# Optimization experiments

Hardware: AMD Instinct MI355X
Metric: run time of the kernel (lower is better)

Reference implementation:

```python
import math
import jax, jax.numpy as jnp
import numpy as np

DEGREE = 5
LN_EPS = 1e-5


def hermite_psi(C, r):
    # x_d = tanh(linspace(-1,1,C)) * (sqrt(2r+1)+1), shape [C]
    x_d = jnp.tanh(jnp.linspace(-1.0, 1.0, C)) * (math.sqrt(2 * r + 1) + 1.0)
    g = jnp.exp(-x_d ** 2 / 2.0)
    rows = [math.pi ** (-0.25) * g]
    if r > 0:
        rows.append(math.sqrt(2.0) * math.pi ** (-0.25) * x_d * g)
    for k in range(2, r + 1):
        rows.append(math.sqrt(2.0 / k) * x_d * rows[-1] - math.sqrt((k - 1) / k) * rows[-2])
    return jnp.stack(rows)  # [r+1, C]


def setup_inputs() -> dict:
    key = jax.random.key(0)
    k1, k2 = jax.random.split(key)
    B, C, H, W = 16, 512, 64, 64
    O = 512
    x = jax.random.normal(k1, (B, C, H, W), dtype=jnp.float32)
    ln_w = jnp.ones((C,), dtype=jnp.float32)
    ln_b = jnp.zeros((C,), dtype=jnp.float32)
    fc_w = jax.random.normal(k2, (O, C), dtype=jnp.float32) * (1.0 / math.sqrt(C))
    fc_b = jnp.zeros((O,), dtype=jnp.float32)
    return {"x": x, "ln_w": ln_w, "ln_b": ln_b, "fc_w": fc_w, "fc_b": fc_b}


def reference(x, ln_w, ln_b, fc_w, fc_b):
    B, C, H, W = x.shape
    O = fc_w.shape[0]
    # [B, HW, C]
    q = x.reshape(B, C, H * W).transpose(0, 2, 1)
    # LayerNorm over channels (biased variance, eps=1e-5)
    mu = q.mean(axis=-1, keepdims=True)
    var = ((q - mu) ** 2).mean(axis=-1, keepdims=True)
    q = (q - mu) / jnp.sqrt(var + LN_EPS) * ln_w + ln_b
    # Constant Hermite basis [r+1, C]
    psi = hermite_psi(C, DEGREE).astype(x.dtype)
    # Tiny cross-attention: scores [B, HW, r+1]
    scores = jnp.einsum('bnc,rc->bnr', q, psi) / math.sqrt(C)
    attn = jax.nn.softmax(scores, axis=-1)
    y = jnp.einsum('bnr,rc->bnc', attn, psi)  # [B, HW, C]
    # 1x1 conv == pointwise GEMM over channels
    out = jnp.einsum('bnc,oc->bon', y, fc_w) + fc_b[None, :, None]
    return out.reshape(B, O, H, W)
```

## Files before the change

kernel.cpp:

```cpp
#include <hip/hip_runtime.h>
#include <math.h>

#define C 512
#define NPIX 4096
#define BATCH 16
#define O 512
#define R 6
#define LN_EPS 1e-5f


__global__ __launch_bounds__(512) void setup_psi(const float* __restrict__ lnw,
                                                 const float* __restrict__ lnb,
                                                 float* __restrict__ ws) {
    __shared__ float sh_psi[R * C];
    const int c = threadIdx.x;
    float t = -1.0f + 2.0f * (float)c / 511.0f;
    float xd = tanhf(t) * 4.31662479035539984911f;
    float g = expf(-0.5f * xd * xd);
    const float pi_m14 = 0.75112554446494248286f;
    float rows[R];
    rows[0] = pi_m14 * g;
    rows[1] = 1.41421356237309504880f * pi_m14 * xd * g;
    #pragma unroll
    for (int k = 2; k <= 5; ++k)
        rows[k] = sqrtf(2.0f / k) * xd * rows[k - 1] - sqrtf((k - 1.0f) / k) * rows[k - 2];
    float w = lnw[c];
    #pragma unroll
    for (int r = 0; r < R; ++r) {
        sh_psi[r * C + c] = rows[r];
        ws[r * C + c] = rows[r];
        ws[3072 + r * C + c] = rows[r] * w;
    }
    __syncthreads();
    if (threadIdx.x < 12) {
        int r = (threadIdx.x < 6) ? threadIdx.x : threadIdx.x - 6;
        const float* vec = (threadIdx.x < 6) ? lnw : lnb;
        float sacc = 0.f;
        for (int c2 = 0; c2 < C; ++c2) sacc += vec[c2] * sh_psi[r * C + c2];
        ws[(threadIdx.x < 6 ? 6144 : 6152) + r] = sacc;
    }
}

__global__ __launch_bounds__(64) void setup_M(const float* __restrict__ fcw,
                                              const float* __restrict__ fcb,
                                              float* __restrict__ ws) {
    const int o = blockIdx.x;
    const int lane = threadIdx.x;
    const float* psi = ws;
    float acc[R] = {0.f, 0.f, 0.f, 0.f, 0.f, 0.f};
    for (int c = lane; c < C; c += 64) {
        float w = fcw[o * C + c];
        #pragma unroll
        for (int r = 0; r < R; ++r) acc[r] += psi[r * C + c] * w;
    }
    #pragma unroll
    for (int r = 0; r < R; ++r)
        for (int m = 32; m >= 1; m >>= 1) acc[r] += __shfl_xor(acc[r], m, 64);
    if (lane == 0) {
        float bias = fcb[o];
        #pragma unroll
        for (int r = 0; r < R; ++r) ws[6160 + r * O + o] = acc[r] + bias;
    }
}

__global__ __launch_bounds__(256) void fused_main(const float* __restrict__ x,
                                                  const float* __restrict__ ws,
                                                  float* __restrict__ out) {
    __shared__ float sh_wpsi[R * C];
    __shared__ float sh_M[R * O];
    const int tid = threadIdx.x;
    const int b = blockIdx.x >> 4;
    const int nblk = blockIdx.x & 15;
    const int n = (nblk << 8) + tid;

    const float* wpsi_g = ws + 3072;
    const float* M_g = ws + 6160;
    for (int i = tid; i < R * C; i += 256) {
        sh_wpsi[i] = wpsi_g[i];
        sh_M[i] = M_g[i];
    }
    float swp[R], sbp[R];
    #pragma unroll
    for (int r = 0; r < R; ++r) { swp[r] = ws[6144 + r]; sbp[r] = ws[6152 + r]; }
    __syncthreads();

    const float* xb = x + (size_t)b * C * NPIX + n;
    float s = 0.f, ss = 0.f;
    float a0 = 0.f, a1 = 0.f, a2 = 0.f, a3 = 0.f, a4 = 0.f, a5 = 0.f;
    #pragma unroll 16
    for (int c = 0; c < C; ++c) {
        float xv = xb[(size_t)c * NPIX];
        s += xv;
        ss += xv * xv;
        a0 += xv * sh_wpsi[0 * C + c];
        a1 += xv * sh_wpsi[1 * C + c];
        a2 += xv * sh_wpsi[2 * C + c];
        a3 += xv * sh_wpsi[3 * C + c];
        a4 += xv * sh_wpsi[4 * C + c];
        a5 += xv * sh_wpsi[5 * C + c];
    }
    float mu = s * (1.0f / 512.0f);
    float var = ss * (1.0f / 512.0f) - mu * mu;
    float rsig = rsqrtf(var + LN_EPS);
    const float invsq = 0.04419417382415922f;

    float a[R] = {a0, a1, a2, a3, a4, a5};
    float sc[R];
    float mx = -1e30f;
    #pragma unroll
    for (int r = 0; r < R; ++r) {
        sc[r] = ((a[r] - mu * swp[r]) * rsig + sbp[r]) * invsq;
        mx = fmaxf(mx, sc[r]);
    }
    float attn[R];
    float es = 0.f;
    #pragma unroll
    for (int r = 0; r < R; ++r) { attn[r] = expf(sc[r] - mx); es += attn[r]; }
    float inv = 1.0f / es;
    #pragma unroll
    for (int r = 0; r < R; ++r) attn[r] *= inv;

    float* ob = out + (size_t)b * O * NPIX + n;
    #pragma unroll 8
    for (int o = 0; o < O; ++o) {
        float v = attn[0] * sh_M[0 * O + o] + attn[1] * sh_M[1 * O + o] +
                  attn[2] * sh_M[2 * O + o] + attn[3] * sh_M[3 * O + o] +
                  attn[4] * sh_M[4 * O + o] + attn[5] * sh_M[5 * O + o];
        ob[(size_t)o * NPIX] = v;
    }
}

extern "C" void kernel_launch(void* const* d_in, const int* in_sizes, int n_in,
                              void* d_out, int out_size, void* d_ws, size_t ws_size,
                              hipStream_t stream) {
    const float* x    = (const float*)d_in[0];
    const float* ln_w = (const float*)d_in[1];
    const float* ln_b = (const float*)d_in[2];
    const float* fc_w = (const float*)d_in[3];
    const float* fc_b = (const float*)d_in[4];
    float* out = (float*)d_out;
    float* ws = (float*)d_ws;

    setup_psi<<<1, 512, 0, stream>>>(ln_w, ln_b, ws);
    setup_M<<<O, 64, 0, stream>>>(fc_w, fc_b, ws);
    fused_main<<<BATCH * 16, 256, 0, stream>>>(x, ws, out);
}
```

Before: 278.3 us.

## Split channel reduction across waves, use more blocks and vectorized float4 stores

The main kernel now runs 1024 blocks of 64 pixels each instead of 256 blocks of 256 pixels. Within a block, the four waves each reduce a quarter of the channels and combine their partial sums through shared memory. The weighted-psi table is stored interleaved per channel so each channel needs one float4 plus one float2 shared-memory load. The output GEMM has each thread write float4 over 4 pixels for 32 output channels. The setup reduction is also parallelized with wave shuffles. The aim is more parallelism for the bandwidth-bound read and write phases, at the cost of extra barriers and shared-memory traffic.

```diff
diff --git a/kernel.cpp b/kernel.cpp
--- a/kernel.cpp
+++ b/kernel.cpp
@@ -28,16 +28,28 @@
     #pragma unroll
     for (int r = 0; r < R; ++r) {
         sh_psi[r * C + c] = rows[r];
-        ws[r * C + c] = rows[r];
-        ws[3072 + r * C + c] = rows[r] * w;
+        ws[8192 + r * C + c] = rows[r];
+        ws[c * 8 + r] = rows[r] * w;
     }
     __syncthreads();
-    if (threadIdx.x < 12) {
-        int r = (threadIdx.x < 6) ? threadIdx.x : threadIdx.x - 6;
-        const float* vec = (threadIdx.x < 6) ? lnw : lnb;
-        float sacc = 0.f;
-        for (int c2 = 0; c2 < C; ++c2) sacc += vec[c2] * sh_psi[r * C + c2];
-        ws[(threadIdx.x < 6 ? 6144 : 6152) + r] = sacc;
+    const int wv = threadIdx.x >> 6;
+    const int l = threadIdx.x & 63;
+    #pragma unroll
+    for (int pass = 0; pass < 2; ++pass) {
+        int combo = pass * 8 + wv;
+        if (combo < 12) {
+            int r = (combo < 6) ? combo : combo - 6;
+            const float* vec = (combo < 6) ? lnw : lnb;
+            float acc = 0.f;
+            #pragma unroll
+            for (int j = 0; j < 8; ++j) {
+                int cc = l + 64 * j;
+                acc += vec[cc] * sh_psi[r * C + cc];
+            }
+            #pragma unroll
+            for (int m = 32; m >= 1; m >>= 1) acc += __shfl_xor(acc, m, 64);
+            if (l == 0) ws[(combo < 6 ? 4096 : 4104) + r] = acc;
+        }
     }
 }
 
@@ -46,7 +58,7 @@
                                               float* __restrict__ ws) {
     const int o = blockIdx.x;
     const int lane = threadIdx.x;
-    const float* psi = ws;
+    const float* psi = ws + 8192;
     float acc[R] = {0.f, 0.f, 0.f, 0.f, 0.f, 0.f};
     for (int c = lane; c < C; c += 64) {
         float w = fcw[o * C + c];
@@ -59,74 +71,101 @@
     if (lane == 0) {
         float bias = fcb[o];
         #pragma unroll
-        for (int r = 0; r < R; ++r) ws[6160 + r * O + o] = acc[r] + bias;
+        for (int r = 0; r < R; ++r) ws[4112 + r * O + o] = acc[r] + bias;
     }
 }
 
-__global__ __launch_bounds__(256) void fused_main(const float* __restrict__ x,
-                                                  const float* __restrict__ ws,
-                                                  float* __restrict__ out) {
-    __shared__ float sh_wpsi[R * C];
-    __shared__ float sh_M[R * O];
+__global__ __launch_bounds__(256, 4) void fused_main(const float* __restrict__ x,
+                                                     const float* __restrict__ ws,
+                                                     float* __restrict__ out) {
+    __shared__ float shW[C * 8];
+    __shared__ float shM[R * O];
+    __shared__ float part[4][8][64];
+    __shared__ float attnS[R][64];
+
     const int tid = threadIdx.x;
-    const int b = blockIdx.x >> 4;
-    const int nblk = blockIdx.x & 15;
-    const int n = (nblk << 8) + tid;
+    const int wv = tid >> 6;
+    const int l = tid & 63;
+    const int b = blockIdx.x >> 6;
+    const int ng = blockIdx.x & 63;
+    const int n0 = ng << 6;
 
-    const float* wpsi_g = ws + 3072;
-    const float* M_g = ws + 6160;
-    for (int i = tid; i < R * C; i += 256) {
-        sh_wpsi[i] = wpsi_g[i];
-        sh_M[i] = M_g[i];
+    {
+        const float4* wsrc = (const float4*)ws;
+        float4* wdst = (float4*)shW;
+        for (int i = tid; i < 1024; i += 256) wdst[i] = wsrc[i];
+        const float4* msrc = (const float4*)(ws + 4112);
+        float4* mdst = (float4*)shM;
+        for (int i = tid; i < 768; i += 256) mdst[i] = msrc[i];
     }
-    float swp[R], sbp[R];
-    #pragma unroll
-    for (int r = 0; r < R; ++r) { swp[r] = ws[6144 + r]; sbp[r] = ws[6152 + r]; }
     __syncthreads();
 
-    const float* xb = x + (size_t)b * C * NPIX + n;
+    const float* xb = x + ((size_t)(b * C + (wv << 7)) << 12) + n0 + l;
     float s = 0.f, ss = 0.f;
     float a0 = 0.f, a1 = 0.f, a2 = 0.f, a3 = 0.f, a4 = 0.f, a5 = 0.f;
     #pragma unroll 16
-    for (int c = 0; c < C; ++c) {
-        float xv = xb[(size_t)c * NPIX];
+    for (int i = 0; i < 128; ++i) {
+        float xv = xb[(size_t)i << 12];
+        const float* wr = &shW[((wv << 7) + i) << 3];
+        float4 w03 = *(const float4*)wr;
+        float2 w45 = *(const float2*)(wr + 4);
         s += xv;
         ss += xv * xv;
-        a0 += xv * sh_wpsi[0 * C + c];
-        a1 += xv * sh_wpsi[1 * C + c];
-        a2 += xv * sh_wpsi[2 * C + c];
-        a3 += xv * sh_wpsi[3 * C + c];
-        a4 += xv * sh_wpsi[4 * C + c];
-        a5 += xv * sh_wpsi[5 * C + c];
+        a0 += xv * w03.x;
+        a1 += xv * w03.y;
+        a2 += xv * w03.z;
+        a3 += xv * w03.w;
+        a4 += xv * w45.x;
+        a5 += xv * w45.y;
     }
-    float mu = s * (1.0f / 512.0f);
-    float var = ss * (1.0f / 512.0f) - mu * mu;
-    float rsig = rsqrtf(var + LN_EPS);
-    const float invsq = 0.04419417382415922f;
+    part[wv][0][l] = s;  part[wv][1][l] = ss;
+    part[wv][2][l] = a0; part[wv][3][l] = a1;
+    part[wv][4][l] = a2; part[wv][5][l] = a3;
+    part[wv][6][l] = a4; part[wv][7][l] = a5;
+    __syncthreads();
 
-    float a[R] = {a0, a1, a2, a3, a4, a5};
-    float sc[R];
-    float mx = -1e30f;
+    if (tid < 64) {
+        float v[8];
+        #pragma unroll
+        for (int j = 0; j < 8; ++j)
+            v[j] = part[0][j][tid] + part[1][j][tid] + part[2][j][tid] + part[3][j][tid];
+        float mu = v[0] * (1.0f / 512.0f);
+        float var = v[1] * (1.0f / 512.0f) - mu * mu;
+        float rsig = rsqrtf(var + LN_EPS);
+        const float invsq = 0.04419417382415922f;
+        float sc[R], mx = -1e30f;
+        #pragma unroll
+        for (int r = 0; r < R; ++r) {
+            float swp = ws[4096 + r], sbp = ws[4104 + r];
+            sc[r] = ((v[2 + r] - mu * swp) * rsig + sbp) * invsq;
+            mx = fmaxf(mx, sc[r]);
+        }
+        float es = 0.f, at[R];
+        #pragma unroll
+        for (int r = 0; r < R; ++r) { at[r] = expf(sc[r] - mx); es += at[r]; }
+        float inv = 1.0f / es;
+        #pragma unroll
+        for (int r = 0; r < R; ++r) attnS[r][tid] = at[r] * inv;
+    }
+    __syncthreads();
+
+    const int pxg = (tid & 15) << 2;
+    const int og = tid >> 4;
+    float4 a4v[R];
     #pragma unroll
-    for (int r = 0; r < R; ++r) {
-        sc[r] = ((a[r] - mu * swp[r]) * rsig + sbp[r]) * invsq;
-        mx = fmaxf(mx, sc[r]);
-    }
-    float attn[R];
-    float es = 0.f;
-    #pragma unroll
-    for (int r = 0; r < R; ++r) { attn[r] = expf(sc[r] - mx); es += attn[r]; }
-    float inv = 1.0f / es;
-    #pragma unroll
-    for (int r = 0; r < R; ++r) attn[r] *= inv;
-
-    float* ob = out + (size_t)b * O * NPIX + n;
+    for (int r = 0; r < R; ++r) a4v[r] = *(const float4*)&attnS[r][pxg];
+    float* ob = out + ((size_t)(b * O) << 12) + n0 + pxg;
     #pragma unroll 8
-    for (int o = 0; o < O; ++o) {
-        float v = attn[0] * sh_M[0 * O + o] + attn[1] * sh_M[1 * O + o] +
-                  attn[2] * sh_M[2 * O + o] + attn[3] * sh_M[3 * O + o] +
-                  attn[4] * sh_M[4 * O + o] + attn[5] * sh_M[5 * O + o];
-        ob[(size_t)o * NPIX] = v;
+    for (int k = 0; k < 32; ++k) {
+        int o = og + (k << 4);
+        float m0 = shM[0 * O + o], m1 = shM[1 * O + o], m2 = shM[2 * O + o];
+        float m3 = shM[3 * O + o], m4 = shM[4 * O + o], m5 = shM[5 * O + o];
+        float4 res;
+        res.x = a4v[0].x * m0 + a4v[1].x * m1 + a4v[2].x * m2 + a4v[3].x * m3 + a4v[4].x * m4 + a4v[5].x * m5;
+        res.y = a4v[0].y * m0 + a4v[1].y * m1 + a4v[2].y * m2 + a4v[3].y * m3 + a4v[4].y * m4 + a4v[5].y * m5;
+        res.z = a4v[0].z * m0 + a4v[1].z * m1 + a4v[2].z * m2 + a4v[3].z * m3 + a4v[4].z * m4 + a4v[5].z * m5;
+        res.w = a4v[0].w * m0 + a4v[1].w * m1 + a4v[2].w * m2 + a4v[3].w * m3 + a4v[4].w * m4 + a4v[5].w * m5;
+        *(float4*)(ob + ((size_t)o << 12)) = res;
     }
 }
 
@@ -143,5 +182,5 @@
 
     setup_psi<<<1, 512, 0, stream>>>(ln_w, ln_b, ws);
     setup_M<<<O, 64, 0, stream>>>(fc_w, fc_b, ws);
-    fused_main<<<BATCH * 16, 256, 0, stream>>>(x, ws, out);
+    fused_main<<<BATCH * 64, 256, 0, stream>>>(x, ws, out);
 }
```

Measured after the change: 272.3 us. 2.2% less time.
